# Kernel tuning notes

Hardware: AMD Instinct MI355X
Metric: run time of the kernel (lower is better)

## Reference

```python
import jax, jax.numpy as jnp
import numpy as np

DIM = 768
HEADS = 12
HEAD_DIM = DIM // HEADS
HIDDEN = 4 * DIM


def layer_norm(x, g, b, eps=1e-5):
    mu = jnp.mean(x, axis=-1, keepdims=True)
    var = jnp.var(x, axis=-1, keepdims=True)
    return (x - mu) * jax.lax.rsqrt(var + eps) * g + b


def setup_inputs() -> dict:
    key = jax.random.key(0)
    ks = jax.random.split(key, 8)
    s = lambda fan_in: 1.0 / np.sqrt(fan_in)
    return {
        "x": jax.random.normal(ks[0], (16, 577, DIM), dtype=jnp.float32),
        "ln1_g": jnp.ones((DIM,), jnp.float32),
        "ln1_b": jnp.zeros((DIM,), jnp.float32),
        "w_qkv": jax.random.uniform(ks[1], (DIM, 3 * DIM), jnp.float32, -s(DIM), s(DIM)),
        "b_qkv": jnp.zeros((3 * DIM,), jnp.float32),
        "w_proj": jax.random.uniform(ks[2], (DIM, DIM), jnp.float32, -s(DIM), s(DIM)),
        "b_proj": jnp.zeros((DIM,), jnp.float32),
        "ln2_g": jnp.ones((DIM,), jnp.float32),
        "ln2_b": jnp.zeros((DIM,), jnp.float32),
        "w_fc1": jax.random.uniform(ks[3], (DIM, HIDDEN), jnp.float32, -s(DIM), s(DIM)),
        "b_fc1": jnp.zeros((HIDDEN,), jnp.float32),
        "w_fc2": jax.random.uniform(ks[4], (HIDDEN, DIM), jnp.float32, -s(HIDDEN), s(HIDDEN)),
        "b_fc2": jnp.zeros((DIM,), jnp.float32),
    }


def reference(x, ln1_g, ln1_b, w_qkv, b_qkv, w_proj, b_proj,
              ln2_g, ln2_b, w_fc1, b_fc1, w_fc2, b_fc2):
    B, N, C = x.shape
    scale = HEAD_DIM ** -0.5

    # --- attention branch (pre-norm) ---
    h = layer_norm(x, ln1_g, ln1_b)
    qkv = h @ w_qkv + b_qkv                               # [B,N,3C]
    qkv = qkv.reshape(B, N, 3, HEADS, HEAD_DIM)
    q, k, v = [qkv[:, :, i].transpose(0, 2, 1, 3) for i in range(3)]  # [B,H,N,D]
    attn = jnp.einsum("bhnd,bhmd->bhnm", q, k) * scale
    attn = jax.nn.softmax(attn, axis=-1)
    out = jnp.einsum("bhnm,bhmd->bhnd", attn, v)          # [B,H,N,D]
    out = out.transpose(0, 2, 1, 3).reshape(B, N, C)
    x = x + (out @ w_proj + b_proj)

    # --- MLP branch (pre-norm) ---
    h = layer_norm(x, ln2_g, ln2_b)
    h = jax.nn.gelu(h @ w_fc1 + b_fc1, approximate=False)
    x = x + (h @ w_fc2 + b_fc2)
    return x
```

## Files before the change

kernel.cpp:

```cpp
#include <hip/hip_runtime.h>
#include <hip/hip_bf16.h>
#include <math.h>

#define NB   16
#define NTOK 577
#define CDIM 768
#define NH   12
#define HID  3072
#define RTOT (NB*NTOK)
#define RPAD (((RTOT+127)/128)*128)
#define BH   (NB*NH)
#define QT   40
#define KF_C (CDIM/32)

typedef __attribute__((ext_vector_type(8))) short bf16x8;
typedef __attribute__((ext_vector_type(4))) float f32x4;
typedef unsigned short u16;

__device__ inline void load_lds16(const void* g, void* l) {
    __builtin_amdgcn_global_load_lds(
        (const __attribute__((address_space(1))) unsigned*)g,
        (__attribute__((address_space(3))) unsigned*)l, 16, 0, 0);
}

__device__ inline size_t blobA(int m, int c, int Kf) {
    return ((size_t)(m >> 4) * Kf + (c >> 5)) * 512 +
           (((c >> 3) & 3) * 16 + (m & 15)) * 8 + (c & 7);
}

__device__ inline float fast_gelu(float x) {
    float y = 0.7978845608f * (x + 0.044715f * x * x * x);
    float e = __expf(2.0f * y);
    float th = 1.0f - 2.0f / (e + 1.0f);
    return 0.5f * x * (1.0f + th);
}

__global__ __launch_bounds__(256) void wconvert_blob(
    const float* __restrict__ src, u16* __restrict__ dst, int K, int N)
{
    int n  = blockIdx.x * 256 + threadIdx.x;
    int kp = blockIdx.y;
    const float* s = src + (size_t)(kp * 8) * N + n;
    __hip_bfloat16 h0 = __float2bfloat16(s[0 * N]);
    __hip_bfloat16 h1 = __float2bfloat16(s[1 * N]);
    __hip_bfloat16 h2 = __float2bfloat16(s[2 * N]);
    __hip_bfloat16 h3 = __float2bfloat16(s[3 * N]);
    __hip_bfloat16 h4 = __float2bfloat16(s[4 * N]);
    __hip_bfloat16 h5 = __float2bfloat16(s[5 * N]);
    __hip_bfloat16 h6 = __float2bfloat16(s[6 * N]);
    __hip_bfloat16 h7 = __float2bfloat16(s[7 * N]);
    ushort4 a = make_ushort4(*(u16*)&h0, *(u16*)&h1, *(u16*)&h2, *(u16*)&h3);
    ushort4 b = make_ushort4(*(u16*)&h4, *(u16*)&h5, *(u16*)&h6, *(u16*)&h7);
    u16* d = dst + ((size_t)(n >> 4) * (K >> 5) + (kp >> 2)) * 512 +
             ((kp & 3) * 16 + (n & 15)) * 8;
    *(ushort4*)(d)     = a;
    *(ushort4*)(d + 4) = b;
}

__global__ __launch_bounds__(256) void ln_kernel(
    const float* __restrict__ x, const float* __restrict__ g,
    const float* __restrict__ b, u16* __restrict__ out)
{
    int row = blockIdx.x;
    const float* xr = x + (size_t)row * CDIM;
    int t = threadIdx.x;
    float v0 = xr[t], v1 = xr[t + 256], v2 = xr[t + 512];
    float s  = v0 + v1 + v2;
    float s2 = v0*v0 + v1*v1 + v2*v2;
    #pragma unroll
    for (int off = 32; off; off >>= 1) {
        s  += __shfl_xor(s, off);
        s2 += __shfl_xor(s2, off);
    }
    __shared__ float red[10];
    int wave = t >> 6, lane = t & 63;
    if (lane == 0) { red[wave] = s; red[wave + 4] = s2; }
    __syncthreads();
    if (t == 0) {
        float ts  = red[0] + red[1] + red[2] + red[3];
        float ts2 = red[4] + red[5] + red[6] + red[7];
        float mu  = ts * (1.0f / CDIM);
        float var = ts2 * (1.0f / CDIM) - mu * mu;
        red[8] = mu;
        red[9] = rsqrtf(var + 1e-5f);
    }
    __syncthreads();
    float mu = red[8], rs = red[9];
    #pragma unroll
    for (int i = 0; i < 3; ++i) {
        int c = t + i * 256;
        float v = (i == 0 ? v0 : (i == 1 ? v1 : v2));
        __hip_bfloat16 hb = __float2bfloat16((v - mu) * rs * g[c] + b[c]);
        out[blobA(row, c, KF_C)] = *(u16*)&hb;
    }
}

template<int MBL, int NBL, int FLAGS>
__global__ __launch_bounds__(256) void tile_gemm(
    const u16* __restrict__ Ab, const u16* __restrict__ Bb,
    const float* __restrict__ bias, const float* __restrict__ res,
    void* __restrict__ outv,
    u16* __restrict__ Qp, u16* __restrict__ Kp, u16* __restrict__ Vp,
    int M, int Nc, int K, int nb, int mtiles)
{
    constexpr int NST  = (MBL + NBL) / 4;
    constexpr int BUFU = (MBL + NBL) * 512;
    constexpr int MH2  = MBL / 2, NW2 = NBL / 2;
    __shared__ __align__(16) u16 smem[2 * BUFU];

    int tid = threadIdx.x, lane = tid & 63, wv = tid >> 6;
    int fr = lane & 15, fq = lane >> 4;
    int wm = wv >> 1, wn = wv & 1;

    int fid = blockIdx.x;
    int xcd = fid & 7, w = fid >> 3;
    int slab = w / nb, n = w - slab * nb;
    int mtile = slab * 8 + xcd;
    if (mtile >= mtiles) return;
    int m0 = mtile * (MBL * 16), n0 = n * (NBL * 16);

    int Kf = K >> 5;
    size_t tstr = (size_t)Kf * 512;

    const u16* gp[NST];
    u16* ldst[NST];
    #pragma unroll
    for (int i = 0; i < NST; ++i) {
        int bi = wv + i * 4;
        gp[i] = (bi < MBL)
            ? Ab + ((size_t)(m0 >> 4) + bi) * tstr + lane * 8
            : Bb + ((size_t)(n0 >> 4) + (bi - MBL)) * tstr + lane * 8;
        ldst[i] = smem + bi * 512;
    }

    f32x4 acc[MH2][NW2];
    #pragma unroll
    for (int mi = 0; mi < MH2; ++mi)
        #pragma unroll
        for (int ni = 0; ni < NW2; ++ni) acc[mi][ni] = (f32x4){0.f, 0.f, 0.f, 0.f};

    #pragma unroll
    for (int i = 0; i < NST; ++i) load_lds16(gp[i], ldst[i]);
    __syncthreads();

    for (int t = 0; t < Kf; ++t) {
        int cur = (t & 1) * BUFU, nxt = ((t + 1) & 1) * BUFU;
        if (t + 1 < Kf) {
            #pragma unroll
            for (int i = 0; i < NST; ++i)
                load_lds16(gp[i] + (size_t)(t + 1) * 512, ldst[i] + nxt);
        }
        bf16x8 a[MH2], bfr[NW2];
        #pragma unroll
        for (int mi = 0; mi < MH2; ++mi)
            a[mi] = *(const bf16x8*)(smem + cur + (wm * MH2 + mi) * 512 + lane * 8);
        #pragma unroll
        for (int ni = 0; ni < NW2; ++ni)
            bfr[ni] = *(const bf16x8*)(smem + cur + (MBL + wn * NW2 + ni) * 512 + lane * 8);
        #pragma unroll
        for (int mi = 0; mi < MH2; ++mi)
            #pragma unroll
            for (int ni = 0; ni < NW2; ++ni)
                acc[mi][ni] = __builtin_amdgcn_mfma_f32_16x16x32_bf16(
                    a[mi], bfr[ni], acc[mi][ni], 0, 0, 0);
        __syncthreads();
    }

    int m0w = m0 + wm * (MH2 * 16);
    int n0w = n0 + wn * (NW2 * 16);
    float* outf = (float*)outv;
    u16* outblob = (u16*)outv;

    if constexpr ((FLAGS & 8) != 0) {
        int sec = n0w / CDIM;
        int h   = (n0w % CDIM) / 64;
        #pragma unroll
        for (int mi = 0; mi < MH2; ++mi) {
            #pragma unroll
            for (int rg = 0; rg < 4; ++rg) {
                int gm = m0w + mi * 16 + fq * 4 + rg;
                if (gm >= M) continue;
                int b   = gm / NTOK;
                int row = gm - b * NTOK;
                int bh  = b * NH + h;
                #pragma unroll
                for (int ni = 0; ni < NW2; ++ni) {
                    int d = ni * 16 + fr;
                    float v = acc[mi][ni][rg] + bias[n0w + d];
                    __hip_bfloat16 hb = __float2bfloat16(v);
                    if (sec == 0) {
                        Qp[(size_t)(bh * QT + (row >> 4)) * 1024 + (d >> 5) * 512 +
                           (((d >> 3) & 3) * 16 + (row & 15)) * 8 + (d & 7)] = *(u16*)&hb;
                    } else if (sec == 1) {
                        Kp[(size_t)(bh * QT + (row >> 4)) * 1024 + (d >> 5) * 512 +
                           (((d >> 3) & 3) * 16 + (row & 15)) * 8 + (d & 7)] = *(u16*)&hb;
                    } else {
                        Vp[((size_t)(bh * 4 + (d >> 4)) * 20 + (row >> 5)) * 512 +
                           (((row >> 3) & 3) * 16 + (d & 15)) * 8 + (row & 7)] = *(u16*)&hb;
                    }
                }
            }
        }
        return;
    }

    if constexpr ((FLAGS & 4) != 0) {
        u16* sb = smem + wv * 1024;
        int KfO = Nc >> 5;
        #pragma unroll
        for (int mi = 0; mi < MH2; ++mi) {
            #pragma unroll
            for (int ni = 0; ni < NW2; ++ni)
                #pragma unroll
                for (int rg = 0; rg < 4; ++rg) {
                    int cl = ni * 16 + fr;
                    float v = acc[mi][ni][rg] + bias[n0w + cl];
                    if (FLAGS & 1) v = fast_gelu(v);
                    __hip_bfloat16 hb = __float2bfloat16(v);
                    sb[(cl >> 5) * 512 +
                       (((cl >> 3) & 3) * 16 + fq * 4 + rg) * 8 + (cl & 7)] = *(u16*)&hb;
                }
            u16* dst = outblob + ((size_t)((m0w >> 4) + mi) * KfO + (n0w >> 5)) * 512;
            *(bf16x8*)(dst + lane * 16)     = *(const bf16x8*)(sb + lane * 16);
            *(bf16x8*)(dst + lane * 16 + 8) = *(const bf16x8*)(sb + lane * 16 + 8);
        }
        return;
    }

    #pragma unroll
    for (int mi = 0; mi < MH2; ++mi) {
        #pragma unroll
        for (int rg = 0; rg < 4; ++rg) {
            int gm = m0w + mi * 16 + fq * 4 + rg;
            if (gm >= M) continue;
            #pragma unroll
            for (int ni = 0; ni < NW2; ++ni) {
                int gn = n0w + ni * 16 + fr;
                float v = acc[mi][ni][rg] + bias[gn];
                if (res) v += res[(size_t)gm * Nc + gn];
                outf[(size_t)gm * Nc + gn] = v;
            }
        }
    }
}

__global__ __launch_bounds__(256) void attn_mfma(
    const u16* __restrict__ Qp, const u16* __restrict__ Kp,
    const u16* __restrict__ Vp, u16* __restrict__ outp)
{
    __shared__ __align__(16) u16 Ks[4096];
    __shared__ __align__(16) u16 Vs[4096];
    __shared__ __align__(16) u16 Ps[4 * 16 * 72];

    int fid = blockIdx.x;
    int xcd = fid & 7, w = fid >> 3;
    int bhl = w / 10, qc = w - bhl * 10;
    int bh = xcd * 24 + bhl;
    int b = bh / NH, h = bh % NH;
    int t = threadIdx.x, lane = t & 63, wv = t >> 6;
    int fr = lane & 15, fq = lane >> 4;

    int mt = qc * 4 + wv;
    const u16* qbase = Qp + (size_t)(bh * QT + mt) * 1024 + lane * 8;
    bf16x8 qf0 = *(const bf16x8*)(qbase);
    bf16x8 qf1 = *(const bf16x8*)(qbase + 512);

    const u16* kg = Kp + (size_t)bh * (QT * 1024) + wv * 1024 + lane * 8;
    const u16* vg = Vp + ((size_t)(bh * 4 + wv) * 20) * 512 + lane * 8;
    u16* lK  = Ks + wv * 1024;
    u16* lV  = Vs + wv * 1024;
    u16* psw = Ps + wv * (16 * 72);

    f32x4 o[4];
    float m_r[4], l_r[4];
    #pragma unroll
    for (int i = 0; i < 4; ++i) {
        o[i] = (f32x4){0.f, 0.f, 0.f, 0.f};
        m_r[i] = -1e30f; l_r[i] = 0.f;
    }

    for (int kt = 0; kt < 10; ++kt) {
        load_lds16(kg + kt * 4096,       lK);
        load_lds16(kg + kt * 4096 + 512, lK + 512);
        load_lds16(vg + kt * 1024,       lV);
        load_lds16(vg + kt * 1024 + 512, lV + 512);
        __syncthreads();

        f32x4 sc[4];
        #pragma unroll
        for (int nt = 0; nt < 4; ++nt) {
            sc[nt] = (f32x4){0.f, 0.f, 0.f, 0.f};
            bf16x8 kf0 = *(const bf16x8*)(Ks + (nt * 2 + 0) * 512 + lane * 8);
            bf16x8 kf1 = *(const bf16x8*)(Ks + (nt * 2 + 1) * 512 + lane * 8);
            sc[nt] = __builtin_amdgcn_mfma_f32_16x16x32_bf16(qf0, kf0, sc[nt], 0, 0, 0);
            sc[nt] = __builtin_amdgcn_mfma_f32_16x16x32_bf16(qf1, kf1, sc[nt], 0, 0, 0);
        }

        int j0 = kt * 64;
        float p[4][4], rm[4];
        #pragma unroll
        for (int rg = 0; rg < 4; ++rg) rm[rg] = -1e30f;
        #pragma unroll
        for (int nt = 0; nt < 4; ++nt) {
            bool valid = (j0 + nt * 16 + fr) < NTOK;
            #pragma unroll
            for (int rg = 0; rg < 4; ++rg) {
                float sv = valid ? sc[nt][rg] * 0.125f : -1e30f;
                p[nt][rg] = sv;
                rm[rg] = fmaxf(rm[rg], sv);
            }
        }
        #pragma unroll
        for (int rg = 0; rg < 4; ++rg) {
            #pragma unroll
            for (int off = 1; off < 16; off <<= 1)
                rm[rg] = fmaxf(rm[rg], __shfl_xor(rm[rg], off));
        }
        float alpha[4], rs[4];
        #pragma unroll
        for (int rg = 0; rg < 4; ++rg) {
            float mn = fmaxf(m_r[rg], rm[rg]);
            alpha[rg] = __expf(m_r[rg] - mn);
            m_r[rg] = mn;
            rs[rg] = 0.f;
        }
        #pragma unroll
        for (int nt = 0; nt < 4; ++nt)
            #pragma unroll
            for (int rg = 0; rg < 4; ++rg) {
                float pv = __expf(p[nt][rg] - m_r[rg]);
                p[nt][rg] = pv;
                rs[rg] += pv;
            }
        #pragma unroll
        for (int rg = 0; rg < 4; ++rg) {
            #pragma unroll
            for (int off = 1; off < 16; off <<= 1)
                rs[rg] += __shfl_xor(rs[rg], off);
            l_r[rg] = l_r[rg] * alpha[rg] + rs[rg];
        }

        #pragma unroll
        for (int nt = 0; nt < 4; ++nt)
            #pragma unroll
            for (int rg = 0; rg < 4; ++rg) {
                __hip_bfloat16 hb = __float2bfloat16(p[nt][rg]);
                psw[(fq * 4 + rg) * 72 + nt * 16 + fr] = *(u16*)&hb;
            }
        #pragma unroll
        for (int dt = 0; dt < 4; ++dt)
            #pragma unroll
            for (int rg = 0; rg < 4; ++rg)
                o[dt][rg] *= alpha[rg];

        bf16x8 pf0 = *(const bf16x8*)(psw + fr * 72 + fq * 8);
        bf16x8 pf1 = *(const bf16x8*)(psw + fr * 72 + 32 + fq * 8);
        #pragma unroll
        for (int dt = 0; dt < 4; ++dt) {
            bf16x8 bv0 = *(const bf16x8*)(Vs + (dt * 2 + 0) * 512 + lane * 8);
            bf16x8 bv1 = *(const bf16x8*)(Vs + (dt * 2 + 1) * 512 + lane * 8);
            o[dt] = __builtin_amdgcn_mfma_f32_16x16x32_bf16(pf0, bv0, o[dt], 0, 0, 0);
            o[dt] = __builtin_amdgcn_mfma_f32_16x16x32_bf16(pf1, bv1, o[dt], 0, 0, 0);
        }
        __syncthreads();
    }

    #pragma unroll
    for (int rg = 0; rg < 4; ++rg) {
        int row = qc * 64 + wv * 16 + fq * 4 + rg;
        if (row < NTOK) {
            float rl = 1.0f / l_r[rg];
            int grow = b * NTOK + row;
            #pragma unroll
            for (int dt = 0; dt < 4; ++dt) {
                __hip_bfloat16 hb = __float2bfloat16(o[dt][rg] * rl);
                outp[blobA(grow, h * 64 + dt * 16 + fr, KF_C)] = *(u16*)&hb;
            }
        }
    }
}

static inline int tg_grid(int nb, int mt) { return 8 * nb * ((mt + 7) / 8); }

extern "C" void kernel_launch(void* const* d_in, const int* in_sizes, int n_in,
                              void* d_out, int out_size, void* d_ws, size_t ws_size,
                              hipStream_t stream)
{
    const float* x      = (const float*)d_in[0];
    const float* ln1_g  = (const float*)d_in[1];
    const float* ln1_b  = (const float*)d_in[2];
    const float* w_qkv  = (const float*)d_in[3];
    const float* b_qkv  = (const float*)d_in[4];
    const float* w_proj = (const float*)d_in[5];
    const float* b_proj = (const float*)d_in[6];
    const float* ln2_g  = (const float*)d_in[7];
    const float* ln2_b  = (const float*)d_in[8];
    const float* w_fc1  = (const float*)d_in[9];
    const float* b_fc1  = (const float*)d_in[10];
    const float* w_fc2  = (const float*)d_in[11];
    const float* b_fc2  = (const float*)d_in[12];
    float* out = (float*)d_out;

    char* w = (char*)d_ws;
    u16* Bqkv = (u16*)w; w += (size_t)3*CDIM*CDIM*2;
    u16* Bproj= (u16*)w; w += (size_t)CDIM*CDIM*2;
    u16* Bfc1 = (u16*)w; w += (size_t)HID*CDIM*2;
    u16* Bfc2 = (u16*)w; w += (size_t)CDIM*HID*2;
    u16* hA   = (u16*)w; w += (size_t)RPAD*CDIM*2;
    u16* h3A  = (u16*)w; w += (size_t)RPAD*HID*2;
    u16* Qp   = (u16*)w; w += (size_t)BH*QT*1024*2;
    u16* Kp   = (u16*)w; w += (size_t)BH*QT*1024*2;
    u16* Vp   = (u16*)w; w += (size_t)BH*4*20*512*2;

    int mt128 = (RTOT + 127) / 128;
    int mt64  = (RTOT + 63) / 64;

    wconvert_blob<<<dim3(3*CDIM/256, CDIM/8), 256, 0, stream>>>(w_qkv,  Bqkv, CDIM, 3*CDIM);
    wconvert_blob<<<dim3(CDIM/256,   CDIM/8), 256, 0, stream>>>(w_proj, Bproj, CDIM, CDIM);
    wconvert_blob<<<dim3(HID/256,    CDIM/8), 256, 0, stream>>>(w_fc1,  Bfc1, CDIM, HID);
    wconvert_blob<<<dim3(CDIM/256,   HID/8),  256, 0, stream>>>(w_fc2,  Bfc2, HID, CDIM);

    ln_kernel<<<RTOT, 256, 0, stream>>>(x, ln1_g, ln1_b, hA);
    tile_gemm<8, 8, 8><<<tg_grid(3*CDIM/128, mt128), 256, 0, stream>>>(
        hA, Bqkv, b_qkv, nullptr, nullptr, Qp, Kp, Vp,
        RTOT, 3*CDIM, CDIM, 3*CDIM/128, mt128);
    attn_mfma<<<8 * 24 * 10, 256, 0, stream>>>(Qp, Kp, Vp, hA);
    tile_gemm<4, 8, 0><<<tg_grid(CDIM/128, mt64), 256, 0, stream>>>(
        hA, Bproj, b_proj, x, out, nullptr, nullptr, nullptr,
        RTOT, CDIM, CDIM, CDIM/128, mt64);
    ln_kernel<<<RTOT, 256, 0, stream>>>(out, ln2_g, ln2_b, hA);
    tile_gemm<8, 8, 5><<<tg_grid(HID/128, mt128), 256, 0, stream>>>(
        hA, Bfc1, b_fc1, nullptr, h3A, nullptr, nullptr, nullptr,
        RTOT, HID, CDIM, HID/128, mt128);
    tile_gemm<4, 8, 0><<<tg_grid(CDIM/128, mt64), 256, 0, stream>>>(
        h3A, Bfc2, b_fc2, out, out, nullptr, nullptr, nullptr,
        RTOT, CDIM, HID, CDIM/128, mt64);
}
```

Baseline: 465.4 us.

## Double-buffer K/V tiles in attention and vectorize LayerNorm stores

The attention kernel now keeps two LDS buffers for K and V and prefetches the next key tile while computing on the current one, so global-to-LDS loads overlap with MFMA work. It also raises wave priority around the MFMA blocks. Separately, LayerNorm stages each normalized row in LDS and writes it out as 16-byte vectors instead of scattered 2-byte stores. The costs are doubled LDS for K/V and an extra barrier in LayerNorm. The prefetch relies on the end-of-iteration barrier for completion, since direct-to-LDS loads need a wait before use, and the attention kernel is only part of the total time.

Result: faster. 451.2 us (-3.1%).

```diff
diff --git a/kernel.cpp b/kernel.cpp
--- a/kernel.cpp
+++ b/kernel.cpp
@@ -73,6 +73,7 @@
         s2 += __shfl_xor(s2, off);
     }
     __shared__ float red[10];
+    __shared__ __align__(16) u16 rowbuf[CDIM];
     int wave = t >> 6, lane = t & 63;
     if (lane == 0) { red[wave] = s; red[wave + 4] = s2; }
     __syncthreads();
@@ -91,7 +92,12 @@
         int c = t + i * 256;
         float v = (i == 0 ? v0 : (i == 1 ? v1 : v2));
         __hip_bfloat16 hb = __float2bfloat16((v - mu) * rs * g[c] + b[c]);
-        out[blobA(row, c, KF_C)] = *(u16*)&hb;
+        rowbuf[c] = *(u16*)&hb;
+    }
+    __syncthreads();
+    if (t < CDIM / 8) {
+        int c0 = t * 8;
+        *(bf16x8*)(out + blobA(row, c0, KF_C)) = *(const bf16x8*)(rowbuf + c0);
     }
 }
 
@@ -248,8 +254,8 @@
     const u16* __restrict__ Qp, const u16* __restrict__ Kp,
     const u16* __restrict__ Vp, u16* __restrict__ outp)
 {
-    __shared__ __align__(16) u16 Ks[4096];
-    __shared__ __align__(16) u16 Vs[4096];
+    __shared__ __align__(16) u16 Ks[2][4096];
+    __shared__ __align__(16) u16 Vs[2][4096];
     __shared__ __align__(16) u16 Ps[4 * 16 * 72];
 
     int fid = blockIdx.x;
@@ -267,9 +273,14 @@
 
     const u16* kg = Kp + (size_t)bh * (QT * 1024) + wv * 1024 + lane * 8;
     const u16* vg = Vp + ((size_t)(bh * 4 + wv) * 20) * 512 + lane * 8;
-    u16* lK  = Ks + wv * 1024;
-    u16* lV  = Vs + wv * 1024;
     u16* psw = Ps + wv * (16 * 72);
+
+#define STAGE(buf, kt) do {                                        \
+    load_lds16(kg + (kt) * 4096,       &Ks[buf][wv * 1024]);       \
+    load_lds16(kg + (kt) * 4096 + 512, &Ks[buf][wv * 1024 + 512]); \
+    load_lds16(vg + (kt) * 1024,       &Vs[buf][wv * 1024]);       \
+    load_lds16(vg + (kt) * 1024 + 512, &Vs[buf][wv * 1024 + 512]); \
+} while (0)
 
     f32x4 o[4];
     float m_r[4], l_r[4];
@@ -279,22 +290,24 @@
         m_r[i] = -1e30f; l_r[i] = 0.f;
     }
 
+    STAGE(0, 0);
+    __syncthreads();
+
     for (int kt = 0; kt < 10; ++kt) {
-        load_lds16(kg + kt * 4096,       lK);
-        load_lds16(kg + kt * 4096 + 512, lK + 512);
-        load_lds16(vg + kt * 1024,       lV);
-        load_lds16(vg + kt * 1024 + 512, lV + 512);
-        __syncthreads();
+        int cur = kt & 1;
+        if (kt + 1 < 10) STAGE(cur ^ 1, kt + 1);
 
         f32x4 sc[4];
+        __builtin_amdgcn_s_setprio(1);
         #pragma unroll
         for (int nt = 0; nt < 4; ++nt) {
             sc[nt] = (f32x4){0.f, 0.f, 0.f, 0.f};
-            bf16x8 kf0 = *(const bf16x8*)(Ks + (nt * 2 + 0) * 512 + lane * 8);
-            bf16x8 kf1 = *(const bf16x8*)(Ks + (nt * 2 + 1) * 512 + lane * 8);
+            bf16x8 kf0 = *(const bf16x8*)(&Ks[cur][(nt * 2 + 0) * 512] + lane * 8);
+            bf16x8 kf1 = *(const bf16x8*)(&Ks[cur][(nt * 2 + 1) * 512] + lane * 8);
             sc[nt] = __builtin_amdgcn_mfma_f32_16x16x32_bf16(qf0, kf0, sc[nt], 0, 0, 0);
             sc[nt] = __builtin_amdgcn_mfma_f32_16x16x32_bf16(qf1, kf1, sc[nt], 0, 0, 0);
         }
+        __builtin_amdgcn_s_setprio(0);
 
         int j0 = kt * 64;
         float p[4][4], rm[4];
@@ -355,15 +368,18 @@
 
         bf16x8 pf0 = *(const bf16x8*)(psw + fr * 72 + fq * 8);
         bf16x8 pf1 = *(const bf16x8*)(psw + fr * 72 + 32 + fq * 8);
+        __builtin_amdgcn_s_setprio(1);
         #pragma unroll
         for (int dt = 0; dt < 4; ++dt) {
-            bf16x8 bv0 = *(const bf16x8*)(Vs + (dt * 2 + 0) * 512 + lane * 8);
-            bf16x8 bv1 = *(const bf16x8*)(Vs + (dt * 2 + 1) * 512 + lane * 8);
+            bf16x8 bv0 = *(const bf16x8*)(&Vs[cur][(dt * 2 + 0) * 512] + lane * 8);
+            bf16x8 bv1 = *(const bf16x8*)(&Vs[cur][(dt * 2 + 1) * 512] + lane * 8);
             o[dt] = __builtin_amdgcn_mfma_f32_16x16x32_bf16(pf0, bv0, o[dt], 0, 0, 0);
             o[dt] = __builtin_amdgcn_mfma_f32_16x16x32_bf16(pf1, bv1, o[dt], 0, 0, 0);
         }
+        __builtin_amdgcn_s_setprio(0);
         __syncthreads();
     }
+#undef STAGE
 
     #pragma unroll
     for (int rg = 0; rg < 4; ++rg) {
```
